# Kernel optimization log

Measured on AMD Instinct MI355X. Metric: run time of the kernel, lower is better.

## Reference

```python
import jax, jax.numpy as jnp
import numpy as np
from jax import lax

N = 20000        # nodes
E = 320000       # directed edges (avg degree 16)
F_IN = 512       # input feature dim
HID = 64         # hidden_layer
K_NEI = 8        # sampled neighbors per node
L = K_NEI + 1    # local subgraph size (self + neighbors)
N_TPL = 10       # N_templates
NT = 8           # N_templates_nodes
N_CLS = 6
ALPHA = 0.5      # FGW trade-off
EPS = 0.1        # entropic regularization
N_OUTER = 3      # outer CG iterations
N_SINK = 5       # sinkhorn iterations per outer step


def setup_inputs() -> dict:
    rng = np.random.default_rng(0)
    src = rng.integers(0, N, E).astype(np.int64)
    dst = rng.integers(0, N, E).astype(np.int64)
    edge_index = np.stack([src, dst])

    # fixed-size neighbor table (pad with self, mask)
    nbr = np.full((N, K_NEI), -1, np.int64)
    cnt = np.zeros(N, np.int64)
    for s, d in zip(src, dst):
        c = cnt[s]
        if c < K_NEI:
            nbr[s, c] = d
            cnt[s] = c + 1
    pad = nbr < 0
    self_col = np.arange(N, dtype=np.int64)
    nbr = np.where(pad, self_col[:, None], nbr)
    nbr_mask = np.concatenate([np.ones((N, 1)), (~pad).astype(np.float64)], 1).astype(np.float32)

    # local adjacency among {self, neighbors}: [N, L, L]
    idx_full = np.concatenate([self_col[:, None], nbr], 1)  # [N, L]
    edge_keys = np.unique(src * N + dst)
    keys = idx_full[:, :, None] * N + idx_full[:, None, :]
    C_local = np.isin(keys, edge_keys).astype(np.float32)

    ks = jax.random.split(jax.random.key(0), 10)
    x = jax.random.normal(ks[0], (N, F_IN), jnp.float32)
    W1 = jax.random.normal(ks[1], (F_IN, HID), jnp.float32) / np.float32(np.sqrt(F_IN))
    b1 = jnp.zeros((HID,), jnp.float32)
    W2 = jax.random.normal(ks[2], (HID, HID), jnp.float32) / np.float32(np.sqrt(HID))
    b2 = jnp.zeros((HID,), jnp.float32)
    t = jax.random.uniform(ks[3], (N_TPL, NT, NT), jnp.float32)
    templates = 0.5 * (t + jnp.swapaxes(t, 1, 2))  # symmetric template adjacency
    templates_features = jax.random.normal(ks[4], (N_TPL, NT, HID), jnp.float32)
    Wlin = jax.random.normal(ks[5], (HID + N_TPL, N_CLS), jnp.float32) / np.float32(np.sqrt(HID + N_TPL))
    blin = jnp.zeros((N_CLS,), jnp.float32)
    return {"x": x, "edge_index": jnp.asarray(edge_index), "nbr_idx": jnp.asarray(nbr),
            "nbr_mask": jnp.asarray(nbr_mask), "C_local": jnp.asarray(C_local),
            "W1": W1, "b1": b1, "W2": W2, "b2": b2,
            "templates": templates, "templates_features": templates_features,
            "Wlin": Wlin, "blin": blin}


def gcn(x, W, b, src, dst, n):
    xw = x @ W
    sl = jnp.arange(n)
    s = jnp.concatenate([src, sl])
    d = jnp.concatenate([dst, sl])
    deg = jax.ops.segment_sum(jnp.ones_like(s, jnp.float32), d, num_segments=n)
    dinv = lax.rsqrt(deg)
    coef = dinv[s] * dinv[d]
    return jax.ops.segment_sum(xw[s] * coef[:, None], d, num_segments=n) + b


def fgw_dist(M, C1, h1, C2, h2):
    # entropic fused GW (square loss) with fixed iterations; padded rows have h1 = 0
    f1 = C1 * C1
    f2 = C2 * C2
    constC = (f1 @ h1)[:, None] + (f2 @ h2)[None, :]
    T0 = h1[:, None] * h2[None, :]

    def outer(T, _):
        tens = constC - 2.0 * (C1 @ T @ C2)
        G = (1.0 - ALPHA) * M + ALPHA * tens
        Kmat = jnp.exp(-G / EPS)

        def sink(carry, _):
            u, v = carry
            u = h1 / (Kmat @ v + 1e-16)
            v = h2 / (Kmat.T @ u + 1e-16)
            return (u, v), None

        (u, v), _ = lax.scan(sink, (jnp.ones_like(h1), jnp.ones_like(h2)), None, length=N_SINK)
        return u[:, None] * Kmat * v[None, :], None

    T, _ = lax.scan(outer, T0, None, length=N_OUTER)
    tens = constC - 2.0 * (C1 @ T @ C2)
    return jnp.sum(T * ((1.0 - ALPHA) * M + ALPHA * tens))


def distance_to_template(x, nbr_idx, nbr_mask, C_local, templates_features, templates):
    n = x.shape[0]
    idx_full = jnp.concatenate([jnp.arange(n)[:, None], nbr_idx], axis=1)  # [N, L]
    xl = x[idx_full]  # [N, L, HID]
    # squared euclidean cost to each template: [N, T, L, NT]
    inner = jnp.einsum('nld,tmd->ntlm', xl, templates_features)
    M = (jnp.sum(xl * xl, -1)[:, None, :, None]
         + jnp.sum(templates_features * templates_features, -1)[None, :, None, :]
         - 2.0 * inner)
    h1 = nbr_mask / jnp.sum(nbr_mask, -1, keepdims=True)  # [N, L]
    h2 = jnp.full((NT,), 1.0 / NT, jnp.float32)

    per_tpl = jax.vmap(fgw_dist, in_axes=(0, None, None, 0, None))
    per_node = jax.vmap(per_tpl, in_axes=(0, 0, 0, None, None))
    return per_node(M, C_local, h1, templates, h2)  # [N, N_TPL]


def reference(x, edge_index, nbr_idx, nbr_mask, C_local, W1, b1, W2, b2,
              templates, templates_features, Wlin, blin):
    src, dst = edge_index[0], edge_index[1]
    n = x.shape[0]
    h = jax.nn.relu(gcn(x, W1, b1, src, dst, n))
    h = gcn(h, W2, b2, src, dst, n)
    y = distance_to_template(h, nbr_idx, nbr_mask, C_local, templates_features, templates)
    out = jnp.concatenate([h, y], axis=1) @ Wlin + blin
    return jax.nn.relu(out)
```

## Files before the change

### kernel.cpp

```cpp
#include <hip/hip_runtime.h>


#define NN   20000
#define EE   320000
#define FIN  512
#define HID  64
#define KNEI 8
#define LSZ  9
#define NTPL 10
#define NTN  8
#define NCLS 6
#define CAP  48

typedef unsigned short bf16_t;
typedef unsigned short us8 __attribute__((ext_vector_type(8)));
typedef __bf16 bf16x8 __attribute__((ext_vector_type(8)));
typedef float f32x4 __attribute__((ext_vector_type(4)));

__device__ __forceinline__ float b2f(bf16_t u) {
  union { unsigned int i; float f; } v; v.i = ((unsigned int)u) << 16; return v.f;
}
__device__ __forceinline__ bf16_t f2b(float f) {
  union { float f; unsigned int i; } v; v.f = f;
  unsigned int x = v.i;
  return (bf16_t)((x + 0x7fffu + ((x >> 16) & 1u)) >> 16);
}
__device__ __forceinline__ float ldf(const void* p, long i, int fp32) {
  return fp32 ? ((const float*)p)[i] : b2f(((const bf16_t*)p)[i]);
}
__device__ __forceinline__ int ldi(const void* p, long i, int i64) {
  return i64 ? (int)((const long long*)p)[i] : ((const int*)p)[i];
}
__device__ __forceinline__ float frcp(float x) { return __builtin_amdgcn_rcpf(x); }

__global__ __launch_bounds__(128) void probe_kernel(const void* __restrict__ x,
                                                    const void* __restrict__ ei,
                                                    const void* __restrict__ tfeat,
                                                    int* __restrict__ flags,
                                                    float* __restrict__ tn2min) {
  __shared__ int sfl[2];
  __shared__ float tn2s[80];
  int tid = threadIdx.x;
  if (tid == 0) {
    int sane = 0;
    for (int k = 0; k < 64; k += 2) {
      bf16_t u = ((const bf16_t*)x)[k];
      int e = (u >> 7) & 0xff;
      if (e >= 112 && e <= 142) sane++;
    }
    int f0 = (sane < 24) ? 1 : 0;
    int zc = 0;
    for (int k = 1; k < 64; k += 2)
      if (((const int*)ei)[k] == 0) zc++;
    int f1 = (zc >= 16) ? 1 : 0;
    flags[0] = f0; flags[1] = f1;
    sfl[0] = f0; sfl[1] = f1;
  }
  __syncthreads();
  if (tid < 80) {
    int fF = sfl[0];
    float s = 0.f;
    for (int k = 0; k < HID; ++k) {
      float v = ldf(tfeat, (long)tid * HID + k, fF);
      s += v * v;
    }
    tn2s[tid] = s;
  }
  __syncthreads();
  if (tid == 0) {
    float gmin = 1e30f;
    for (int t = 0; t < NTPL; ++t) {
      float m = tn2s[t * 8];
      for (int r = 1; r < 8; ++r) m = fminf(m, tn2s[t * 8 + r]);
      tn2min[t] = m;
      gmin = fminf(gmin, m);
    }
    tn2min[NTPL] = gmin;
  }
}

__global__ __launch_bounds__(256) void scatter_kernel(const void* __restrict__ ei,
                                                      int* __restrict__ pos,
                                                      int* __restrict__ slot,
                                                      const int* __restrict__ flags) {
  int i = blockIdx.x * 256 + threadIdx.x;
  if (i >= EE) return;
  int i64 = flags[1];
  int s = ldi(ei, i, i64);
  int d = ldi(ei, (long)EE + i, i64);
  int p = atomicAdd(&pos[d], 1);
  if (p < CAP) slot[d * CAP + p] = s;
}

__global__ __launch_bounds__(256) void wt_kernel(const void* __restrict__ W1,
                                                 bf16_t* __restrict__ w1t,
                                                 const int* __restrict__ flags) {
  if (flags[0]) return;
  __shared__ bf16_t tile[HID][HID + 2];
  const int b = blockIdx.x;
  const int tid = threadIdx.x;
  const bf16_t* w = (const bf16_t*)W1;
  for (int i = tid; i < 512; i += 256) {
    int kk = i >> 3, c8 = i & 7;
    us8 v = *(const us8*)&w[(long)(64 * b + kk) * HID + c8 * 8];
#pragma unroll
    for (int q = 0; q < 8; ++q) tile[c8 * 8 + q][kk] = v[q];
  }
  __syncthreads();
  for (int i = tid; i < 512; i += 256) {
    int c = i >> 3, j = i & 7;
    us8 v;
#pragma unroll
    for (int q = 0; q < 8; ++q) v[q] = tile[c][j * 8 + q];
    *(us8*)&w1t[(long)c * FIN + 64 * b + j * 8] = v;
  }
}

__global__ __launch_bounds__(256, 2) void gemm1_kernel(const void* __restrict__ x,
                                                       const bf16_t* __restrict__ w1t,
                                                       const void* __restrict__ W1,
                                                       float* __restrict__ xw1,
                                                       const int* __restrict__ flags) {
  const int tid = threadIdx.x;
  const int wid = tid >> 6;
  const int lane = tid & 63;

  if (!flags[0]) {
    const int ct = wid;
    const int lr = lane & 15;
    const int lg = lane >> 4;
    const int row = blockIdx.x * 16 + lr;
    const bf16x8* xp = (const bf16x8*)x + (long)row * (FIN / 8) + lg;
    const bf16x8* ap = (const bf16x8*)w1t + (long)(ct * 16 + lr) * (FIN / 8) + lg;
    f32x4 acc0 = {0.f, 0.f, 0.f, 0.f};
    f32x4 acc1 = {0.f, 0.f, 0.f, 0.f};
#pragma unroll
    for (int s = 0; s < 16; s += 2) {
      bf16x8 a0 = ap[4 * s];
      bf16x8 b0 = xp[4 * s];
      bf16x8 a1 = ap[4 * s + 4];
      bf16x8 b1 = xp[4 * s + 4];
      acc0 = __builtin_amdgcn_mfma_f32_16x16x32_bf16(a0, b0, acc0, 0, 0, 0);
      acc1 = __builtin_amdgcn_mfma_f32_16x16x32_bf16(a1, b1, acc1, 0, 0, 0);
    }
    f32x4 r = acc0 + acc1;
    *(f32x4*)&xw1[(long)row * HID + ct * 16 + lg * 4] = r;
  } else {
    int row0 = (blockIdx.x * 4 + wid) * 4;
    if (row0 >= NN) return;
    float a0 = 0.f, a1 = 0.f, a2 = 0.f, a3 = 0.f;
    const float* x0 = (const float*)x + (long)row0 * FIN;
    const float* wp = (const float*)W1;
#pragma unroll 8
    for (int k = 0; k < FIN; ++k) {
      float w = wp[k * HID + lane];
      a0 += x0[k] * w;
      a1 += x0[FIN + k] * w;
      a2 += x0[2 * FIN + k] * w;
      a3 += x0[3 * FIN + k] * w;
    }
    xw1[(long)(row0 + 0) * HID + lane] = a0;
    xw1[(long)(row0 + 1) * HID + lane] = a1;
    xw1[(long)(row0 + 2) * HID + lane] = a2;
    xw1[(long)(row0 + 3) * HID + lane] = a3;
  }
}

__global__ __launch_bounds__(256) void gatherA_kernel(const float* __restrict__ xw,
                                                      const int* __restrict__ cnt,
                                                      const int* __restrict__ slot,
                                                      float* __restrict__ xw2,
                                                      const void* __restrict__ b1v,
                                                      const void* __restrict__ W2,
                                                      const int* __restrict__ flags) {
  int n = blockIdx.x * 4 + (threadIdx.x >> 6);
  if (n >= NN) return;
  int fF = flags[0];
  int c = threadIdx.x & 63;
  float dn = rsqrtf((float)cnt[n] + 1.0f);
  float acc = xw[(long)n * HID + c] * dn;
  int m = cnt[n]; if (m > CAP) m = CAP;
  const int* sl = slot + (long)n * CAP;
  float accB = 0.f;
  for (int e0 = 0; e0 < m; e0 += 8) {
    int4 sa = *(const int4*)(sl + e0);
    int4 sb = *(const int4*)(sl + e0 + 4);
    if (e0 + 0 < m) acc  += xw[(long)sa.x * HID + c] * rsqrtf((float)cnt[sa.x] + 1.0f);
    if (e0 + 1 < m) accB += xw[(long)sa.y * HID + c] * rsqrtf((float)cnt[sa.y] + 1.0f);
    if (e0 + 2 < m) acc  += xw[(long)sa.z * HID + c] * rsqrtf((float)cnt[sa.z] + 1.0f);
    if (e0 + 3 < m) accB += xw[(long)sa.w * HID + c] * rsqrtf((float)cnt[sa.w] + 1.0f);
    if (e0 + 4 < m) acc  += xw[(long)sb.x * HID + c] * rsqrtf((float)cnt[sb.x] + 1.0f);
    if (e0 + 5 < m) accB += xw[(long)sb.y * HID + c] * rsqrtf((float)cnt[sb.y] + 1.0f);
    if (e0 + 6 < m) acc  += xw[(long)sb.z * HID + c] * rsqrtf((float)cnt[sb.z] + 1.0f);
    if (e0 + 7 < m) accB += xw[(long)sb.w * HID + c] * rsqrtf((float)cnt[sb.w] + 1.0f);
  }
  float h1 = (acc + accB) * dn + ldf(b1v, c, fF);
  h1 = h1 > 0.f ? h1 : 0.f;

  float o = 0.f;
#pragma unroll 8
  for (int k = 0; k < HID; ++k)
    o += __shfl(h1, k) * ldf(W2, k * HID + c, fF);
  xw2[(long)n * HID + c] = o;
}

__global__ __launch_bounds__(256) void gatherB_kernel(const float* __restrict__ xw,
                                                      const int* __restrict__ cnt,
                                                      const int* __restrict__ slot,
                                                      float* __restrict__ h,
                                                      float* __restrict__ n2,
                                                      const void* __restrict__ b2v,
                                                      const int* __restrict__ flags) {
  int n = blockIdx.x * 4 + (threadIdx.x >> 6);
  if (n >= NN) return;
  int c = threadIdx.x & 63;
  float dn = rsqrtf((float)cnt[n] + 1.0f);
  float acc = xw[(long)n * HID + c] * dn;
  int m = cnt[n]; if (m > CAP) m = CAP;
  const int* sl = slot + (long)n * CAP;
  float accB = 0.f;
  for (int e0 = 0; e0 < m; e0 += 8) {
    int4 sa = *(const int4*)(sl + e0);
    int4 sb = *(const int4*)(sl + e0 + 4);
    if (e0 + 0 < m) acc  += xw[(long)sa.x * HID + c] * rsqrtf((float)cnt[sa.x] + 1.0f);
    if (e0 + 1 < m) accB += xw[(long)sa.y * HID + c] * rsqrtf((float)cnt[sa.y] + 1.0f);
    if (e0 + 2 < m) acc  += xw[(long)sa.z * HID + c] * rsqrtf((float)cnt[sa.z] + 1.0f);
    if (e0 + 3 < m) accB += xw[(long)sa.w * HID + c] * rsqrtf((float)cnt[sa.w] + 1.0f);
    if (e0 + 4 < m) acc  += xw[(long)sb.x * HID + c] * rsqrtf((float)cnt[sb.x] + 1.0f);
    if (e0 + 5 < m) accB += xw[(long)sb.y * HID + c] * rsqrtf((float)cnt[sb.y] + 1.0f);
    if (e0 + 6 < m) acc  += xw[(long)sb.z * HID + c] * rsqrtf((float)cnt[sb.z] + 1.0f);
    if (e0 + 7 < m) accB += xw[(long)sb.w * HID + c] * rsqrtf((float)cnt[sb.w] + 1.0f);
  }
  acc = (acc + accB) * dn;
  h[(long)n * HID + c] = acc;
  float v = acc + ldf(b2v, c, flags[0]);
  float s = v * v;
  s += __shfl_xor(s, 1); s += __shfl_xor(s, 2); s += __shfl_xor(s, 4);
  s += __shfl_xor(s, 8); s += __shfl_xor(s, 16); s += __shfl_xor(s, 32);
  if (c == 0) n2[n] = s;
}

#define NODES_PB 4
#define TPN 80
#define XLP 65

__global__ __launch_bounds__(320, 2) void fgw_kernel(
    const float* __restrict__ h2,
    const void* __restrict__ b2v,
    const void* __restrict__ nbr_idx,
    const void* __restrict__ nbr_mask,
    const void* __restrict__ C_local,
    const void* __restrict__ tmpl,
    const void* __restrict__ tfeat,
    const void* __restrict__ Wlin,
    const void* __restrict__ blin,
    void* __restrict__ out,
    const int* __restrict__ flags,
    const float* __restrict__ tn2min,
    const float* __restrict__ n2)
{
  const int tid = threadIdx.x;
  const int fF = flags[0];
  const int fI = flags[1];
  const int nb = tid / TPN;
  const int local = tid - nb * TPN;
  const int t = local >> 3;
  const int j = local & 7;
  const int n = blockIdx.x * NODES_PB + nb;
  const int lane = tid & 63;
  const int ob = lane & 56;

  __shared__ float xlS[NODES_PB][LSZ][XLP];
  __shared__ float C1S[NODES_PB][81];
  __shared__ float hwS[NODES_PB][LSZ];
  __shared__ float f1S[NODES_PB][LSZ];
  __shared__ float xnS[NODES_PB][LSZ];
  __shared__ float distS[NODES_PB][NTPL];
  __shared__ float xmaxS[NODES_PB];
  __shared__ int   needS[NODES_PB];
  __shared__ int   sidxS[NODES_PB][LSZ];
  __shared__ float WlinS[(HID + NTPL) * NCLS + NCLS];

  for (int i = tid; i < (HID + NTPL) * NCLS; i += 320)
    WlinS[i] = ldf(Wlin, i, fF);
  if (tid < NCLS) WlinS[(HID + NTPL) * NCLS + tid] = ldf(blin, tid, fF);

  if (local < LSZ) {
    int idx = (local == 0) ? n : ldi(nbr_idx, (long)n * KNEI + local - 1, fI);
    sidxS[nb][local] = idx;
    xnS[nb][local] = n2[idx];
  }
  if (local < HID)
    xlS[nb][0][local] = h2[(long)n * HID + local] + ldf(b2v, local, fF);
  __syncthreads();

  if (local == 0) {
    float xm = xnS[nb][0];
#pragma unroll
    for (int l = 1; l < LSZ; ++l) xm = fmaxf(xm, xnS[nb][l]);
    xmaxS[nb] = xm;
    needS[nb] = ((sqrtf(tn2min[NTPL]) - sqrtf(xm)) >= 5.0990195f) ? 0 : 1;
  }
  __syncthreads();

  const int need = needS[nb];
  if (need) {
    for (int i = local; i < 8 * HID; i += TPN) {
      int l = 1 + (i >> 6), k = i & 63;
      xlS[nb][l][k] = h2[(long)sidxS[nb][l] * HID + k] + ldf(b2v, k, fF);
    }
    for (int i = local; i < 81; i += TPN)
      C1S[nb][i] = ldf(C_local, (long)n * 81 + i, fF);
  }
  __syncthreads();

  if (need && local < LSZ) {
    int l = local;
    float msum = 0.f, f1 = 0.f;
#pragma unroll
    for (int jj = 0; jj < LSZ; ++jj) {
      float mj = ldf(nbr_mask, (long)n * LSZ + jj, fF);
      msum += mj;
      float c = C1S[nb][l * LSZ + jj];
      f1 += c * c * mj;
    }
    float inv = frcp(msum);
    hwS[nb][l] = ldf(nbr_mask, (long)n * LSZ + l, fF) * inv;
    f1S[nb][l] = f1 * inv;
  }
  __syncthreads();

  bool slow = need && ((sqrtf(tn2min[t]) - sqrtf(xmaxS[nb])) < 5.0990195f);
  if (slow) {
    float C2c[NTN];
    float f2h2;
    {
      float s = 0.f;
#pragma unroll
      for (int m = 0; m < NTN; ++m) {
        C2c[m] = ldf(tmpl, t * 64 + m * 8 + j, fF);
        float r = ldf(tmpl, t * 64 + j * 8 + m, fF);
        s += r * r;
      }
      f2h2 = s * 0.125f;
    }
    float hwr[LSZ], f1r[LSZ];
#pragma unroll
    for (int l = 0; l < LSZ; ++l) { hwr[l] = hwS[nb][l]; f1r[l] = f1S[nb][l]; }

    float Mc[LSZ];
    {
      float accI[LSZ];
#pragma unroll
      for (int l = 0; l < LSZ; ++l) accI[l] = 0.f;
      float tn2 = 0.f;
      const long tb = (long)local * HID;
      for (int kb = 0; kb < 8; ++kb) {
        float r[8];
#pragma unroll
        for (int q = 0; q < 8; ++q) r[q] = ldf(tfeat, tb + kb * 8 + q, fF);
#pragma unroll
        for (int q = 0; q < 8; ++q) tn2 += r[q] * r[q];
#pragma unroll
        for (int l = 0; l < LSZ; ++l) {
          float s = 0.f;
#pragma unroll
          for (int q = 0; q < 8; ++q) s += xlS[nb][l][kb * 8 + q] * r[q];
          accI[l] += s;
        }
      }
#pragma unroll
      for (int l = 0; l < LSZ; ++l)
        Mc[l] = xnS[nb][l] + tn2 - 2.f * accI[l];
    }

    float Tc[LSZ], Kc[LSZ], u[LSZ];
#pragma unroll
    for (int l = 0; l < LSZ; ++l) Tc[l] = hwr[l] * 0.125f;

    float v = 1.0f;
    for (int outer = 0; outer < 3; ++outer) {
      float Ac[LSZ];
#pragma unroll
      for (int l = 0; l < LSZ; ++l) {
        float s = 0.f;
#pragma unroll
        for (int l2 = 0; l2 < LSZ; ++l2) s += C1S[nb][l * LSZ + l2] * Tc[l2];
        Ac[l] = s;
      }
#pragma unroll
      for (int l = 0; l < LSZ; ++l) {
        float s = 0.f;
#pragma unroll
        for (int m = 0; m < NTN; ++m) s += __shfl(Ac[l], ob + m) * C2c[m];
        float tens = f1r[l] + f2h2 - 2.f * s;
        Kc[l] = __expf(-5.0f * (Mc[l] + tens));
      }
      v = 1.0f;
      for (int it = 0; it < 5; ++it) {
#pragma unroll
        for (int l = 0; l < LSZ; ++l) {
          float p = Kc[l] * v;
          p += __shfl_xor(p, 1); p += __shfl_xor(p, 2); p += __shfl_xor(p, 4);
          u[l] = hwr[l] * frcp(p + 1e-16f);
        }
        float s = 0.f;
#pragma unroll
        for (int l = 0; l < LSZ; ++l) s += Kc[l] * u[l];
        v = 0.125f * frcp(s + 1e-16f);
      }
#pragma unroll
      for (int l = 0; l < LSZ; ++l) Tc[l] = u[l] * Kc[l] * v;
    }
    {
      float Ac[LSZ];
#pragma unroll
      for (int l = 0; l < LSZ; ++l) {
        float s = 0.f;
#pragma unroll
        for (int l2 = 0; l2 < LSZ; ++l2) s += C1S[nb][l * LSZ + l2] * Tc[l2];
        Ac[l] = s;
      }
      float cl = 0.f;
#pragma unroll
      for (int l = 0; l < LSZ; ++l) {
        float s = 0.f;
#pragma unroll
        for (int m = 0; m < NTN; ++m) s += __shfl(Ac[l], ob + m) * C2c[m];
        float tens = f1r[l] + f2h2 - 2.f * s;
        cl += Tc[l] * 0.5f * (Mc[l] + tens);
      }
      cl += __shfl_xor(cl, 1); cl += __shfl_xor(cl, 2); cl += __shfl_xor(cl, 4);
      if (j == 0) distS[nb][t] = cl;
    }
  } else if (j == 0) {
    distS[nb][t] = 0.f;
  }
  __syncthreads();

  if (local < NCLS) {
    int c = local;
    float acc = WlinS[(HID + NTPL) * NCLS + c];
#pragma unroll
    for (int k = 0; k < HID; ++k)
      acc += xlS[nb][0][k] * WlinS[k * NCLS + c];
#pragma unroll
    for (int tt = 0; tt < NTPL; ++tt)
      acc += distS[nb][tt] * WlinS[(HID + tt) * NCLS + c];
    float r = acc > 0.f ? acc : 0.f;
    if (fF) ((float*)out)[(long)n * NCLS + c] = r;
    else    ((bf16_t*)out)[(long)n * NCLS + c] = f2b(r);
  }
}

extern "C" void kernel_launch(void* const* d_in, const int* in_sizes, int n_in,
                              void* d_out, int out_size, void* d_ws, size_t ws_size,
                              hipStream_t stream) {
  (void)in_sizes; (void)n_in; (void)out_size; (void)ws_size;
  const void* x     = d_in[0];
  const void* ei    = d_in[1];
  const void* nbr   = d_in[2];
  const void* nmask = d_in[3];
  const void* Cl    = d_in[4];
  const void* W1    = d_in[5];
  const void* b1    = d_in[6];
  const void* W2    = d_in[7];
  const void* b2    = d_in[8];
  const void* tmpl  = d_in[9];
  const void* tfeat = d_in[10];
  const void* Wlin  = d_in[11];
  const void* blin  = d_in[12];

  int*    flags  = (int*)d_ws;
  float*  tn2min = (float*)d_ws + 4;
  float*  n2     = (float*)d_ws + 16;
  int*    pos    = (int*)(n2 + NN);
  int*    slot   = pos + NN;
  float*  bufA   = (float*)(slot + (long)CAP * NN);
  float*  bufB   = bufA + (long)NN * HID;
  bf16_t* w1t    = (bf16_t*)(bufB + (long)NN * HID);

  probe_kernel<<<1, 128, 0, stream>>>(x, ei, tfeat, flags, tn2min);

  hipMemsetAsync(pos, 0, NN * sizeof(int), stream);
  wt_kernel<<<8, 256, 0, stream>>>(W1, w1t, flags);
  scatter_kernel<<<(EE + 255) / 256, 256, 0, stream>>>(ei, pos, slot, flags);

  gemm1_kernel<<<NN / 16, 256, 0, stream>>>(x, w1t, W1, bufA, flags);
  gatherA_kernel<<<NN / 4, 256, 0, stream>>>(bufA, pos, slot, bufB, b1, W2, flags);
  gatherB_kernel<<<NN / 4, 256, 0, stream>>>(bufB, pos, slot, bufA, n2, b2, flags);

  fgw_kernel<<<NN / NODES_PB, 320, 0, stream>>>(bufA, b2, nbr, nmask, Cl, tmpl,
                                                tfeat, Wlin, blin, d_out, flags,
                                                tn2min, n2);
}
```

Before: 315.8 us.

## Stage 32-row x tile in LDS and compute two column tiles per wave in GEMM1

The first-layer GEMM now stages a 32-row block of bf16 input features in padded shared memory. Each wave computes two 16-column output tiles for 16 rows, reusing each x fragment across both tiles. Previously every wave re-read the same x rows from global memory, so this cuts redundant global reads of x and halves the grid. In exchange it adds about 33 KB of LDS per block and drops the 2-blocks-per-SM launch bound hint, which may lower occupancy.

```diff
diff --git a/kernel.cpp b/kernel.cpp
--- a/kernel.cpp
+++ b/kernel.cpp
@@ -11,6 +11,9 @@
 #define NTN  8
 #define NCLS 6
 #define CAP  48
+
+#define XROWS 32
+#define XPAD  520
 
 typedef unsigned short bf16_t;
 typedef unsigned short us8 __attribute__((ext_vector_type(8)));
@@ -116,53 +119,77 @@
   }
 }
 
-__global__ __launch_bounds__(256, 2) void gemm1_kernel(const void* __restrict__ x,
-                                                       const bf16_t* __restrict__ w1t,
-                                                       const void* __restrict__ W1,
-                                                       float* __restrict__ xw1,
-                                                       const int* __restrict__ flags) {
+__global__ __launch_bounds__(256) void gemm1_kernel(const void* __restrict__ x,
+                                                    const bf16_t* __restrict__ w1t,
+                                                    const void* __restrict__ W1,
+                                                    float* __restrict__ xw1,
+                                                    const int* __restrict__ flags) {
   const int tid = threadIdx.x;
   const int wid = tid >> 6;
   const int lane = tid & 63;
 
   if (!flags[0]) {
-    const int ct = wid;
+    __shared__ bf16_t xt[XROWS * XPAD];
+    const bf16_t* xb = (const bf16_t*)x + (long)blockIdx.x * XROWS * FIN;
+#pragma unroll
+    for (int it = 0; it < (XROWS * FIN / 8) / 256; ++it) {
+      int c = it * 256 + tid;
+      int r = c >> 6, cc = c & 63;
+      us8 v = *(const us8*)(xb + r * FIN + cc * 8);
+      *(us8*)&xt[r * XPAD + cc * 8] = v;
+    }
+    __syncthreads();
+
+    const int half = (wid & 1) * 16;
+    const int ct0 = (wid >> 1) * 2;
     const int lr = lane & 15;
     const int lg = lane >> 4;
-    const int row = blockIdx.x * 16 + lr;
-    const bf16x8* xp = (const bf16x8*)x + (long)row * (FIN / 8) + lg;
-    const bf16x8* ap = (const bf16x8*)w1t + (long)(ct * 16 + lr) * (FIN / 8) + lg;
-    f32x4 acc0 = {0.f, 0.f, 0.f, 0.f};
-    f32x4 acc1 = {0.f, 0.f, 0.f, 0.f};
+    const bf16_t* xrow = &xt[(half + lr) * XPAD];
+    const bf16x8* ap0 = (const bf16x8*)w1t + (long)((ct0 + 0) * 16 + lr) * (FIN / 8) + lg;
+    const bf16x8* ap1 = (const bf16x8*)w1t + (long)((ct0 + 1) * 16 + lr) * (FIN / 8) + lg;
+
+    f32x4 acc00 = {0.f, 0.f, 0.f, 0.f};
+    f32x4 acc01 = {0.f, 0.f, 0.f, 0.f};
+    f32x4 acc10 = {0.f, 0.f, 0.f, 0.f};
+    f32x4 acc11 = {0.f, 0.f, 0.f, 0.f};
 #pragma unroll
     for (int s = 0; s < 16; s += 2) {
-      bf16x8 a0 = ap[4 * s];
-      bf16x8 b0 = xp[4 * s];
-      bf16x8 a1 = ap[4 * s + 4];
-      bf16x8 b1 = xp[4 * s + 4];
-      acc0 = __builtin_amdgcn_mfma_f32_16x16x32_bf16(a0, b0, acc0, 0, 0, 0);
-      acc1 = __builtin_amdgcn_mfma_f32_16x16x32_bf16(a1, b1, acc1, 0, 0, 0);
-    }
-    f32x4 r = acc0 + acc1;
-    *(f32x4*)&xw1[(long)row * HID + ct * 16 + lg * 4] = r;
+      bf16x8 b0 = *(const bf16x8*)&xrow[s * 32 + lg * 8];
+      bf16x8 b1 = *(const bf16x8*)&xrow[(s + 1) * 32 + lg * 8];
+      bf16x8 a00 = ap0[4 * s];
+      bf16x8 a10 = ap1[4 * s];
+      bf16x8 a01 = ap0[4 * s + 4];
+      bf16x8 a11 = ap1[4 * s + 4];
+      acc00 = __builtin_amdgcn_mfma_f32_16x16x32_bf16(a00, b0, acc00, 0, 0, 0);
+      acc10 = __builtin_amdgcn_mfma_f32_16x16x32_bf16(a10, b0, acc10, 0, 0, 0);
+      acc01 = __builtin_amdgcn_mfma_f32_16x16x32_bf16(a01, b1, acc01, 0, 0, 0);
+      acc11 = __builtin_amdgcn_mfma_f32_16x16x32_bf16(a11, b1, acc11, 0, 0, 0);
+    }
+    f32x4 r0 = acc00 + acc01;
+    f32x4 r1 = acc10 + acc11;
+    const long grow = (long)blockIdx.x * XROWS + half + lr;
+    *(f32x4*)&xw1[grow * HID + (ct0 + 0) * 16 + lg * 4] = r0;
+    *(f32x4*)&xw1[grow * HID + (ct0 + 1) * 16 + lg * 4] = r1;
   } else {
-    int row0 = (blockIdx.x * 4 + wid) * 4;
-    if (row0 >= NN) return;
-    float a0 = 0.f, a1 = 0.f, a2 = 0.f, a3 = 0.f;
-    const float* x0 = (const float*)x + (long)row0 * FIN;
-    const float* wp = (const float*)W1;
+    for (int g = 0; g < 2; ++g) {
+      int row0 = blockIdx.x * XROWS + wid * 8 + g * 4;
+      if (row0 >= NN) return;
+      float a0 = 0.f, a1 = 0.f, a2 = 0.f, a3 = 0.f;
+      const float* x0 = (const float*)x + (long)row0 * FIN;
+      const float* wp = (const float*)W1;
 #pragma unroll 8
-    for (int k = 0; k < FIN; ++k) {
-      float w = wp[k * HID + lane];
-      a0 += x0[k] * w;
-      a1 += x0[FIN + k] * w;
-      a2 += x0[2 * FIN + k] * w;
-      a3 += x0[3 * FIN + k] * w;
-    }
-    xw1[(long)(row0 + 0) * HID + lane] = a0;
-    xw1[(long)(row0 + 1) * HID + lane] = a1;
-    xw1[(long)(row0 + 2) * HID + lane] = a2;
-    xw1[(long)(row0 + 3) * HID + lane] = a3;
+      for (int k = 0; k < FIN; ++k) {
+        float w = wp[k * HID + lane];
+        a0 += x0[k] * w;
+        a1 += x0[FIN + k] * w;
+        a2 += x0[2 * FIN + k] * w;
+        a3 += x0[3 * FIN + k] * w;
+      }
+      xw1[(long)(row0 + 0) * HID + lane] = a0;
+      xw1[(long)(row0 + 1) * HID + lane] = a1;
+      xw1[(long)(row0 + 2) * HID + lane] = a2;
+      xw1[(long)(row0 + 3) * HID + lane] = a3;
+    }
   }
 }
 
@@ -486,7 +513,7 @@
   wt_kernel<<<8, 256, 0, stream>>>(W1, w1t, flags);
   scatter_kernel<<<(EE + 255) / 256, 256, 0, stream>>>(ei, pos, slot, flags);
 
-  gemm1_kernel<<<NN / 16, 256, 0, stream>>>(x, w1t, W1, bufA, flags);
+  gemm1_kernel<<<NN / XROWS, 256, 0, stream>>>(x, w1t, W1, bufA, flags);
   gatherA_kernel<<<NN / 4, 256, 0, stream>>>(bufA, pos, slot, bufB, b1, W2, flags);
   gatherB_kernel<<<NN / 4, 256, 0, stream>>>(bufB, pos, slot, bufA, n2, b2, flags);
 
```

Measured after the change: 340.2 us. 7.7% more time.
